# Performance work log

Measured on AMD Instinct MI355X. Metric: run time of the kernel, lower is better.

The kernel has to match this reference:

```python
import jax, jax.numpy as jnp
from jax import lax
import numpy as np

NPOINT = 1024   # S: number of sampled centroids
NSAMPLE = 32    # K: neighbors per centroid (unmasked ball query = k-nearest via argsort)


def _gather(p, i):
    # p: [B,N,C], i: [B,...] int -> [B,...,C]
    return jax.vmap(lambda pb, ib: pb[ib])(p, i)


def _fps(xyz, farthest_init, npoint):
    # Iterative farthest point sampling, faithful to the torch loop.
    B, N, _ = xyz.shape
    dist0 = jnp.full((B, N), 1e10, dtype=xyz.dtype)

    def step(carry, _):
        distance, farthest = carry
        centroid = jnp.take_along_axis(xyz, farthest[:, None, None], axis=1)  # [B,1,3]
        d = jnp.sum((xyz - centroid) ** 2, -1)          # [B,N]
        distance = jnp.minimum(distance, d)
        return (distance, jnp.argmax(distance, -1)), farthest

    _, cent = lax.scan(step, (dist0, farthest_init.astype(jnp.int32)), None, length=npoint)
    return cent.T  # [B, npoint]


def _sq_dist(src, dst):
    # src: [B,S,3], dst: [B,N,3] -> [B,S,N]
    return (jnp.sum(src ** 2, -1)[:, :, None]
            + jnp.sum(dst ** 2, -1)[:, None, :]
            - 2.0 * jnp.einsum('bsc,bnc->bsn', src, dst))


def setup_inputs() -> dict:
    key = jax.random.key(0)
    ks = jax.random.split(key, 6)
    B, N, C = 8, 4096, 6
    inp = {
        'xyz': jax.random.normal(ks[0], (B, N, 3), jnp.float32),
        'points': jax.random.normal(ks[1], (B, N, C), jnp.float32),
        'farthest_init': jax.random.randint(ks[2], (B,), 0, N),
    }
    dims = [C + 3, 64, 64, 128]
    for li in range(3):
        inp[f'w{li}'] = jax.random.normal(ks[3 + li], (dims[li + 1], dims[li]), jnp.float32) * 0.1
        inp[f'b{li}'] = jnp.zeros((dims[li + 1],), jnp.float32)
    return inp


def reference(xyz, points, farthest_init, w0, b0, w1, b1, w2, b2):
    fps_idx = _fps(xyz, farthest_init, NPOINT)            # [B,S]
    new_xyz = _gather(xyz, fps_idx)                       # [B,S,3]
    dist = _sq_dist(new_xyz, xyz)                         # [B,S,N]
    _, idx = lax.top_k(-dist, NSAMPLE)                    # k-nearest == argsort[:, :, :K]
    g_xyz = _gather(xyz, idx) - new_xyz[:, :, None, :]    # [B,S,K,3]
    g_pts = _gather(points, idx)                          # [B,S,K,C]
    h = jnp.concatenate([g_xyz, g_pts], axis=-1)          # [B,S,K,C+3]
    for w, b in ((w0, b0), (w1, b1), (w2, b2)):           # 1x1 conv MLP + relu
        h = jax.nn.relu(jnp.einsum('bskc,oc->bsko', h, w) + b)
    new_points = jnp.max(h, axis=2)                       # max-pool over K -> [B,S,128]
    return new_xyz, new_points
```

## Files before the change

### kernel.cpp

```cpp
#include <hip/hip_runtime.h>

#define INF_F 3.402823466e+38f
typedef unsigned long long u64;
typedef __attribute__((ext_vector_type(2))) float f32x2;

__device__ __forceinline__ float f_add(float a, float b){ return __fadd_rn(a,b); }
__device__ __forceinline__ float f_sub(float a, float b){ return __fsub_rn(a,b); }
__device__ __forceinline__ float f_mul(float a, float b){ return __fmul_rn(a,b); }

__device__ __forceinline__ f32x2 pk_add(f32x2 a, f32x2 b){ f32x2 d; asm("v_pk_add_f32 %0, %1, %2" : "=v"(d) : "v"(a), "v"(b)); return d; }
__device__ __forceinline__ f32x2 pk_mul(f32x2 a, f32x2 b){ f32x2 d; asm("v_pk_mul_f32 %0, %1, %2" : "=v"(d) : "v"(a), "v"(b)); return d; }
__device__ __forceinline__ f32x2 pk_fma(f32x2 a, f32x2 b, f32x2 c){ f32x2 d; asm("v_pk_fma_f32 %0, %1, %2, %3" : "=v"(d) : "v"(a), "v"(b), "v"(c)); return d; }

template<int CTRL>
__device__ __forceinline__ double dpp_d(double x) {
    u64 u = (u64)__double_as_longlong(x);
    int lo = __builtin_amdgcn_update_dpp(0, (int)(unsigned)u,        CTRL, 0xF, 0xF, true);
    int hi = __builtin_amdgcn_update_dpp(0, (int)(unsigned)(u>>32), CTRL, 0xF, 0xF, true);
    return __longlong_as_double((long long)(((u64)(unsigned)hi << 32) | (unsigned)lo));
}
template<int CTRL>
__device__ __forceinline__ float dpp_f(float x) {
    int r = __builtin_amdgcn_update_dpp(0, __float_as_int(x), CTRL, 0xF, 0xF, true);
    return __int_as_float(r);
}
__device__ __forceinline__ float swz16_f(float x) {
    return __int_as_float(__builtin_amdgcn_ds_swizzle(__float_as_int(x), 0x401F));
}
__device__ __forceinline__ double readlane_d(double x, int l) {
    u64 u = (u64)__double_as_longlong(x);
    int lo = __builtin_amdgcn_readlane((int)(unsigned)u,        l);
    int hi = __builtin_amdgcn_readlane((int)(unsigned)(u>>32), l);
    return __longlong_as_double((long long)(((u64)(unsigned)hi << 32) | (unsigned)lo));
}
__device__ __forceinline__ unsigned key_lo(double k) {
    return (unsigned)((u64)__double_as_longlong(k) & 0xFFFFFFFFull);
}
__device__ __forceinline__ double pack_key(float nd, unsigned low) {
    return __longlong_as_double((long long)(((u64)__float_as_uint(nd) << 32) | (u64)low));
}

__device__ __forceinline__ double wave_max_key(double k) {
    k = fmax(k, dpp_d<0xB1>(k));
    k = fmax(k, dpp_d<0x4E>(k));
    k = fmax(k, dpp_d<0x141>(k));
    k = fmax(k, dpp_d<0x140>(k));
    double a = readlane_d(k, 0),  b = readlane_d(k, 16);
    double c = readlane_d(k, 32), d = readlane_d(k, 48);
    return fmax(fmax(a, b), fmax(c, d));
}
__device__ __forceinline__ double wave_min_key(double k) {
    k = fmin(k, dpp_d<0xB1>(k));
    k = fmin(k, dpp_d<0x4E>(k));
    k = fmin(k, dpp_d<0x141>(k));
    k = fmin(k, dpp_d<0x140>(k));
    double a = readlane_d(k, 0),  b = readlane_d(k, 16);
    double c = readlane_d(k, 32), d = readlane_d(k, 48);
    return fmin(fmin(a, b), fmin(c, d));
}

__global__ __launch_bounds__(512, 1) void fps8_kernel(
    const float* __restrict__ xyz, const int* __restrict__ farthest_init,
    float* __restrict__ out_new_xyz)
{
    const int b    = blockIdx.x;
    const int tid  = threadIdx.x;
    const int lane = tid & 63;
    const int wid  = tid >> 6;

    __shared__ float4 sp[4096];
    __shared__ int    hist[1024];
    __shared__ double red[2][8];

    const float* xb = xyz + (size_t)b * 4096 * 3;
    for (int n = tid; n < 4096; n += 512)
        sp[n] = make_float4(xb[n*3+0], xb[n*3+1], xb[n*3+2], 0.0f);
    __syncthreads();

    f32x2 px[4], py[4], pz[4], d2a[4];
    #pragma unroll
    for (int jp = 0; jp < 4; ++jp) {
        const int n0 = (2*jp)*512 + tid, n1 = n0 + 512;
        float4 a = sp[n0], c = sp[n1];
        px[jp] = (f32x2){a.x, c.x};
        py[jp] = (f32x2){a.y, c.y};
        pz[jp] = (f32x2){a.z, c.z};
        d2a[jp] = (f32x2){1e10f, 1e10f};
    }

    int far = farthest_init[b];
    float4 cen = sp[far];
    float cx = cen.x, cy = cen.y, cz = cen.z;
    int p = 0;

    #pragma unroll 1
    for (int it = 0; it < 1024; ++it) {
        if (tid == 0) hist[it] = far;
        const f32x2 ncx = (f32x2){-cx, -cx};
        const f32x2 ncy = (f32x2){-cy, -cy};
        const f32x2 ncz = (f32x2){-cz, -cz};

        float nd[8];
        #pragma unroll
        for (int jp = 0; jp < 4; ++jp) {
            f32x2 dx = pk_add(px[jp], ncx);
            f32x2 dy = pk_add(py[jp], ncy);
            f32x2 dz = pk_add(pz[jp], ncz);
            f32x2 d2 = pk_add(pk_add(pk_mul(dx,dx), pk_mul(dy,dy)), pk_mul(dz,dz));
            float a0 = fminf(d2a[jp][0], d2[0]);
            float a1 = fminf(d2a[jp][1], d2[1]);
            d2a[jp][0] = a0; d2a[jp][1] = a1;
            nd[2*jp+0] = a0;
            nd[2*jp+1] = a1;
        }
        float vmax = fmaxf(fmaxf(fmaxf(nd[0], nd[1]), fmaxf(nd[2], nd[3])),
                           fmaxf(fmaxf(nd[4], nd[5]), fmaxf(nd[6], nd[7])));
        unsigned bestn = 0xFFFFFFFFu;
        #pragma unroll
        for (int j = 0; j < 8; ++j) {
            unsigned nj = (unsigned)(j*512 + tid);
            bestn = min(bestn, (nd[j] == vmax) ? nj : 0xFFFFFFFFu);
        }
        double wkey = wave_max_key(pack_key(vmax, 4095u - bestn));
        if (lane == 0) red[p][wid] = wkey;
        __syncthreads();
        const double g = fmax(fmax(fmax(red[p][0], red[p][1]), fmax(red[p][2], red[p][3])),
                              fmax(fmax(red[p][4], red[p][5]), fmax(red[p][6], red[p][7])));
        far = 4095 - (int)key_lo(g);
        float4 cc = sp[far];
        cx = cc.x; cy = cc.y; cz = cc.z;
        p ^= 1;
    }
    __syncthreads();
    #pragma unroll
    for (int q = 0; q < 2; ++q) {
        int s = q * 512 + tid;
        float4 cc = sp[hist[s]];
        float* o = out_new_xyz + ((size_t)b * 1024 + s) * 3;
        o[0] = cc.x; o[1] = cc.y; o[2] = cc.z;
    }
}

template<int G>
__device__ __forceinline__ double rebuild8(const double (&key)[64], double w) {
    const double DINF = __builtin_huge_val();
    double m = DINF;
    #pragma unroll
    for (int e = 0; e < 8; ++e) {
        double v = key[G*8+e];
        v = (v > w) ? v : DINF;
        m = fmin(m, v);
    }
    return m;
}

__global__ __launch_bounds__(256, 1) void knn_kernel(
    const float* __restrict__ xyz, const float* __restrict__ new_xyz,
    int* __restrict__ out_idx)
{
    const int tid  = threadIdx.x;
    const int lane = tid & 63;
    const int wid  = tid >> 6;
    const int blk  = blockIdx.x * 4 + wid;
    const int b    = blk >> 10;

    const float* xb = xyz + (size_t)b * 4096 * 3;
    const float* cp = new_xyz + (size_t)blk * 3;
    const float cx = cp[0], cy = cp[1], cz = cp[2];
    const float src2 = f_add(f_add(f_mul(cx,cx), f_mul(cy,cy)), f_mul(cz,cz));

    double key[64];
    #pragma unroll
    for (int j = 0; j < 64; ++j) {
        const int n = j * 64 + lane;
        const float* pt = xb + n * 3;
        float x = pt[0], y = pt[1], z = pt[2];
        float dst2 = f_add(f_add(f_mul(x,x), f_mul(y,y)), f_mul(z,z));
        float dot  = f_add(f_add(f_mul(cx,x), f_mul(cy,y)), f_mul(cz,z));
        float d = f_sub(f_add(src2, dst2), f_mul(2.0f, dot));
        key[j] = __longlong_as_double((long long)(((u64)__float_as_uint(d) << 32) | (u64)(unsigned)n));
    }

    double gm[8];
    #pragma unroll
    for (int g = 0; g < 8; ++g) {
        double m = key[g*8];
        #pragma unroll
        for (int e = 1; e < 8; ++e) m = fmin(m, key[g*8+e]);
        gm[g] = m;
    }

    double w = -1.0;
    int myidx = 0;
    #pragma unroll 1
    for (int t = 0; t < 32; ++t) {
        double lm = fmin(fmin(fmin(gm[0], gm[1]), fmin(gm[2], gm[3])),
                         fmin(fmin(gm[4], gm[5]), fmin(gm[6], gm[7])));
        double gmin = wave_min_key(lm);
        int n = (int)(unsigned)((u64)__double_as_longlong(gmin) & 0xFFFFFFFFull);
        if (lane == t) myidx = n;
        w = gmin;
        const int gs = __builtin_amdgcn_readfirstlane(n >> 9);
        switch (gs) {
            case 0: gm[0] = rebuild8<0>(key, w); break;
            case 1: gm[1] = rebuild8<1>(key, w); break;
            case 2: gm[2] = rebuild8<2>(key, w); break;
            case 3: gm[3] = rebuild8<3>(key, w); break;
            case 4: gm[4] = rebuild8<4>(key, w); break;
            case 5: gm[5] = rebuild8<5>(key, w); break;
            case 6: gm[6] = rebuild8<6>(key, w); break;
            case 7: gm[7] = rebuild8<7>(key, w); break;
        }
    }
    if (lane < 32) out_idx[(size_t)blk * 32 + lane] = myidx;
}

__global__ __launch_bounds__(256, 1) void mlp_kernel(
    const float* __restrict__ xyz, const float* __restrict__ points,
    const int* __restrict__ knn_idx,
    const float* __restrict__ w0, const float* __restrict__ b0,
    const float* __restrict__ w1, const float* __restrict__ b1,
    const float* __restrict__ w2, const float* __restrict__ b2,
    const float* __restrict__ new_xyz, float* __restrict__ out_np)
{
    const int tid = threadIdx.x;
    const int k   = tid & 31;
    const int gs  = blockIdx.x * 8 + (tid >> 5);
    const int b   = gs >> 10;
    const int n   = knn_idx[(size_t)gs * 32 + k];

    const float cx = new_xyz[gs*3+0], cy = new_xyz[gs*3+1], cz = new_xyz[gs*3+2];
    const float* pxyz = xyz + ((size_t)b * 4096 + n) * 3;
    float h0[9];
    h0[0] = pxyz[0] - cx;
    h0[1] = pxyz[1] - cy;
    h0[2] = pxyz[2] - cz;
    const float* pp = points + ((size_t)b * 4096 + n) * 6;
    #pragma unroll
    for (int c = 0; c < 6; ++c) h0[3 + c] = pp[c];

    f32x2 h1p[32];
    #pragma unroll
    for (int o = 0; o < 64; o += 2) {
        float accA = b0[o], accB = b0[o+1];
        #pragma unroll
        for (int c = 0; c < 9; ++c) {
            accA = fmaf(h0[c], w0[o*9+c],     accA);
            accB = fmaf(h0[c], w0[(o+1)*9+c], accB);
        }
        h1p[o>>1] = (f32x2){fmaxf(accA, 0.0f), fmaxf(accB, 0.0f)};
    }

    const f32x2* w1v = (const f32x2*)w1;
    f32x2 h2p[32];
    #pragma unroll
    for (int o = 0; o < 64; o += 2) {
        f32x2 accA = (f32x2){b1[o],   0.0f};
        f32x2 accB = (f32x2){b1[o+1], 0.0f};
        #pragma unroll
        for (int i = 0; i < 32; ++i) {
            accA = pk_fma(h1p[i], w1v[o*32+i],     accA);
            accB = pk_fma(h1p[i], w1v[(o+1)*32+i], accB);
        }
        h2p[o>>1] = (f32x2){fmaxf(accA[0]+accA[1], 0.0f), fmaxf(accB[0]+accB[1], 0.0f)};
    }

    const f32x2* w2v = (const f32x2*)w2;
    float* outp = out_np + (size_t)gs * 128;
    for (int og = 0; og < 4; ++og) {
        float keep = 0.0f;
        for (int o2 = 0; o2 < 32; ++o2) {
            const int o = og * 32 + o2;
            f32x2 acc = (f32x2){b2[o], 0.0f};
            #pragma unroll
            for (int i = 0; i < 32; ++i) acc = pk_fma(h2p[i], w2v[o*32+i], acc);
            float m = fmaxf(acc[0] + acc[1], 0.0f);
            m = fmaxf(m, dpp_f<0xB1>(m));
            m = fmaxf(m, dpp_f<0x4E>(m));
            m = fmaxf(m, dpp_f<0x141>(m));
            m = fmaxf(m, dpp_f<0x140>(m));
            m = fmaxf(m, swz16_f(m));
            keep = (k == o2) ? m : keep;
        }
        outp[og * 32 + k] = keep;
    }
}

__global__ __launch_bounds__(256) void knn_mlp_kernel(
    const float* __restrict__ xyz, const float* __restrict__ points,
    const float* __restrict__ w0, const float* __restrict__ b0,
    const float* __restrict__ w1, const float* __restrict__ b1,
    const float* __restrict__ w2, const float* __restrict__ b2,
    const float* __restrict__ new_xyz, float* __restrict__ out_np)
{
    const int blk    = blockIdx.x;
    const int b      = blk >> 7;
    const int s_base = (blk & 127) * 8;
    const int tid    = threadIdx.x;
    const int lane   = tid & 63;
    const int wid    = tid >> 6;

    __shared__ float sx[4096], sy[4096], sz[4096];
    __shared__ float cent[8][3];
    __shared__ int   idxbuf[8][32];

    const float* xb = xyz + (size_t)b * 4096 * 3;
    for (int n = tid; n < 4096; n += 256) {
        sx[n] = xb[n*3+0]; sy[n] = xb[n*3+1]; sz[n] = xb[n*3+2];
    }
    if (tid < 24) ((float*)cent)[tid] = new_xyz[((size_t)b * 1024 + s_base) * 3 + tid];
    __syncthreads();

    for (int si = 0; si < 2; ++si) {
        const int sl = wid * 2 + si;
        const float cx = cent[sl][0], cy = cent[sl][1], cz = cent[sl][2];
        const float src2 = f_add(f_add(f_mul(cx,cx), f_mul(cy,cy)), f_mul(cz,cz));
        float d[64];
        #pragma unroll
        for (int j = 0; j < 64; ++j) {
            int n = j * 64 + lane;
            float x = sx[n], y = sy[n], z = sz[n];
            float dst2 = f_add(f_add(f_mul(x,x), f_mul(y,y)), f_mul(z,z));
            float dot  = f_add(f_add(f_mul(cx,x), f_mul(cy,y)), f_mul(cz,z));
            d[j] = f_sub(f_add(src2, dst2), f_mul(2.0f, dot));
        }
        int myg  = 0;
        int prev = -1;
        for (int t = 0; t < 32; ++t) {
            float bv = INF_F; int bi = 0x7fffffff;
            #pragma unroll
            for (int j = 0; j < 64; ++j) {
                int n = j * 64 + lane;
                if (n == prev) d[j] = INF_F;
                float v = d[j];
                if (v < bv) { bv = v; bi = n; }
            }
            #pragma unroll
            for (int m = 1; m < 64; m <<= 1) {
                float ov = __shfl_xor(bv, m);
                int   oi = __shfl_xor(bi, m);
                if (ov < bv || (ov == bv && oi < bi)) { bv = ov; bi = oi; }
            }
            if (lane == t) myg = bi;
            prev = bi;
        }
        if (lane < 32) idxbuf[sl][lane] = myg;
    }
    __syncthreads();

    const int k   = tid & 31;
    const int sl2 = tid >> 5;
    const int s   = s_base + sl2;
    const int n   = idxbuf[sl2][k];

    const float cx = cent[sl2][0], cy = cent[sl2][1], cz = cent[sl2][2];
    float h0[9];
    h0[0] = sx[n] - cx;
    h0[1] = sy[n] - cy;
    h0[2] = sz[n] - cz;
    const float* pp = points + ((size_t)b * 4096 + n) * 6;
    #pragma unroll
    for (int c = 0; c < 6; ++c) h0[3 + c] = pp[c];

    float h1[64];
    #pragma unroll
    for (int o = 0; o < 64; ++o) {
        float acc = b0[o];
        #pragma unroll
        for (int c = 0; c < 9; ++c) acc = fmaf(h0[c], w0[o*9+c], acc);
        h1[o] = fmaxf(acc, 0.0f);
    }
    float h2[64];
    #pragma unroll
    for (int o = 0; o < 64; ++o) {
        float acc = b1[o];
        #pragma unroll
        for (int c = 0; c < 64; ++c) acc = fmaf(h1[c], w1[o*64+c], acc);
        h2[o] = fmaxf(acc, 0.0f);
    }
    float* outp = out_np + ((size_t)b * 1024 + s) * 128;
    for (int og = 0; og < 4; ++og) {
        float keep = 0.0f;
        for (int o2 = 0; o2 < 32; ++o2) {
            const int o = og * 32 + o2;
            float acc = b2[o];
            #pragma unroll
            for (int c = 0; c < 64; ++c) acc = fmaf(h2[c], w2[o*64+c], acc);
            float m = fmaxf(acc, 0.0f);
            #pragma unroll
            for (int mm = 1; mm < 32; mm <<= 1)
                m = fmaxf(m, __shfl_xor(m, mm));
            keep = (k == o2) ? m : keep;
        }
        outp[og * 32 + k] = keep;
    }
}

extern "C" void kernel_launch(void* const* d_in, const int* in_sizes, int n_in,
                              void* d_out, int out_size, void* d_ws, size_t ws_size,
                              hipStream_t stream) {
    const float* xyz           = (const float*)d_in[0];
    const float* points        = (const float*)d_in[1];
    const int*   farthest_init = (const int*)  d_in[2];
    const float* w0 = (const float*)d_in[3];
    const float* b0 = (const float*)d_in[4];
    const float* w1 = (const float*)d_in[5];
    const float* b1 = (const float*)d_in[6];
    const float* w2 = (const float*)d_in[7];
    const float* b2 = (const float*)d_in[8];

    float* out        = (float*)d_out;
    float* new_xyz    = out;
    float* new_points = out + 8 * 1024 * 3;

    fps8_kernel<<<8, 512, 0, stream>>>(xyz, farthest_init, new_xyz);

    if (ws_size >= (size_t)(8192 * 32 * sizeof(int))) {
        int* knn_idx = (int*)d_ws;
        knn_kernel<<<2048, 256, 0, stream>>>(xyz, new_xyz, knn_idx);
        mlp_kernel<<<1024, 256, 0, stream>>>(xyz, points, knn_idx,
                                             w0, b0, w1, b1, w2, b2,
                                             new_xyz, new_points);
    } else {
        knn_mlp_kernel<<<1024, 256, 0, stream>>>(xyz, points, w0, b0, w1, b1, w2, b2,
                                                 new_xyz, new_points);
    }
}
```

Baseline: 881.2 us.

## Replace FPS per-iteration barrier with LDS spin-wait slots and 4 waves

Reworks the farthest point sampling kernel to run 4 waves of 256 threads, each holding 16 points, instead of 8 waves of 512. The per-iteration __syncthreads reduction is replaced by a per-iteration LDS slot array, pre-filled with a poison value, that each wave polls until all four wave maxima are published. The aim is to remove block-barrier latency from the serial 1024-step loop. In exchange each thread carries more registers and ALU work per step, and correctness depends on LDS visibility ordering under volatile spinning with no fences, plus the poison value never colliding with a real key.

```diff
diff --git a/kernel.cpp b/kernel.cpp
--- a/kernel.cpp
+++ b/kernel.cpp
@@ -3,6 +3,8 @@
 #define INF_F 3.402823466e+38f
 typedef unsigned long long u64;
 typedef __attribute__((ext_vector_type(2))) float f32x2;
+
+#define SLOT_POISON 0xAAAAAAAAAAAAAAAAull
 
 __device__ __forceinline__ float f_add(float a, float b){ return __fadd_rn(a,b); }
 __device__ __forceinline__ float f_sub(float a, float b){ return __fsub_rn(a,b); }
@@ -59,7 +61,7 @@
     return fmin(fmin(a, b), fmin(c, d));
 }
 
-__global__ __launch_bounds__(512, 1) void fps8_kernel(
+__global__ __launch_bounds__(256, 1) void fps_spin_kernel(
     const float* __restrict__ xyz, const int* __restrict__ farthest_init,
     float* __restrict__ out_new_xyz)
 {
@@ -70,17 +72,18 @@
 
     __shared__ float4 sp[4096];
     __shared__ int    hist[1024];
-    __shared__ double red[2][8];
+    __shared__ u64    slot[1024][4];
 
     const float* xb = xyz + (size_t)b * 4096 * 3;
-    for (int n = tid; n < 4096; n += 512)
+    for (int n = tid; n < 4096; n += 256)
         sp[n] = make_float4(xb[n*3+0], xb[n*3+1], xb[n*3+2], 0.0f);
+    for (int i = tid; i < 4096; i += 256) ((u64*)slot)[i] = SLOT_POISON;
     __syncthreads();
 
-    f32x2 px[4], py[4], pz[4], d2a[4];
-    #pragma unroll
-    for (int jp = 0; jp < 4; ++jp) {
-        const int n0 = (2*jp)*512 + tid, n1 = n0 + 512;
+    f32x2 px[8], py[8], pz[8], d2a[8];
+    #pragma unroll
+    for (int jp = 0; jp < 8; ++jp) {
+        const int n0 = (2*jp)*256 + tid, n1 = n0 + 256;
         float4 a = sp[n0], c = sp[n1];
         px[jp] = (f32x2){a.x, c.x};
         py[jp] = (f32x2){a.y, c.y};
@@ -91,7 +94,6 @@
     int far = farthest_init[b];
     float4 cen = sp[far];
     float cx = cen.x, cy = cen.y, cz = cen.z;
-    int p = 0;
 
     #pragma unroll 1
     for (int it = 0; it < 1024; ++it) {
@@ -100,9 +102,9 @@
         const f32x2 ncy = (f32x2){-cy, -cy};
         const f32x2 ncz = (f32x2){-cz, -cz};
 
-        float nd[8];
-        #pragma unroll
-        for (int jp = 0; jp < 4; ++jp) {
+        float nd[16];
+        #pragma unroll
+        for (int jp = 0; jp < 8; ++jp) {
             f32x2 dx = pk_add(px[jp], ncx);
             f32x2 dy = pk_add(py[jp], ncy);
             f32x2 dz = pk_add(pz[jp], ncz);
@@ -113,30 +115,41 @@
             nd[2*jp+0] = a0;
             nd[2*jp+1] = a1;
         }
-        float vmax = fmaxf(fmaxf(fmaxf(nd[0], nd[1]), fmaxf(nd[2], nd[3])),
-                           fmaxf(fmaxf(nd[4], nd[5]), fmaxf(nd[6], nd[7])));
+        float m01 = fmaxf(nd[0], nd[1]),   m23 = fmaxf(nd[2], nd[3]);
+        float m45 = fmaxf(nd[4], nd[5]),   m67 = fmaxf(nd[6], nd[7]);
+        float m89 = fmaxf(nd[8], nd[9]),   mAB = fmaxf(nd[10], nd[11]);
+        float mCD = fmaxf(nd[12], nd[13]), mEF = fmaxf(nd[14], nd[15]);
+        float vmax = fmaxf(fmaxf(fmaxf(m01, m23), fmaxf(m45, m67)),
+                           fmaxf(fmaxf(m89, mAB), fmaxf(mCD, mEF)));
         unsigned bestn = 0xFFFFFFFFu;
         #pragma unroll
-        for (int j = 0; j < 8; ++j) {
-            unsigned nj = (unsigned)(j*512 + tid);
+        for (int j = 0; j < 16; ++j) {
+            unsigned nj = (unsigned)(j*256 + tid);
             bestn = min(bestn, (nd[j] == vmax) ? nj : 0xFFFFFFFFu);
         }
         double wkey = wave_max_key(pack_key(vmax, 4095u - bestn));
-        if (lane == 0) red[p][wid] = wkey;
-        __syncthreads();
-        const double g = fmax(fmax(fmax(red[p][0], red[p][1]), fmax(red[p][2], red[p][3])),
-                              fmax(fmax(red[p][4], red[p][5]), fmax(red[p][6], red[p][7])));
+
+        if (lane == 0) slot[it][wid] = (u64)__double_as_longlong(wkey);
+        volatile const u64* s = &slot[it][0];
+        u64 k0, k1, k2, k3;
+        do {
+            k0 = s[0]; k1 = s[1]; k2 = s[2]; k3 = s[3];
+        } while (k0 == SLOT_POISON || k1 == SLOT_POISON ||
+                 k2 == SLOT_POISON || k3 == SLOT_POISON);
+        const double g = fmax(fmax(__longlong_as_double((long long)k0),
+                                   __longlong_as_double((long long)k1)),
+                              fmax(__longlong_as_double((long long)k2),
+                                   __longlong_as_double((long long)k3)));
         far = 4095 - (int)key_lo(g);
         float4 cc = sp[far];
         cx = cc.x; cy = cc.y; cz = cc.z;
-        p ^= 1;
     }
     __syncthreads();
     #pragma unroll
-    for (int q = 0; q < 2; ++q) {
-        int s = q * 512 + tid;
-        float4 cc = sp[hist[s]];
-        float* o = out_new_xyz + ((size_t)b * 1024 + s) * 3;
+    for (int q = 0; q < 4; ++q) {
+        int s2 = q * 256 + tid;
+        float4 cc = sp[hist[s2]];
+        float* o = out_new_xyz + ((size_t)b * 1024 + s2) * 3;
         o[0] = cc.x; o[1] = cc.y; o[2] = cc.z;
     }
 }
@@ -413,7 +426,7 @@
     float* new_xyz    = out;
     float* new_points = out + 8 * 1024 * 3;
 
-    fps8_kernel<<<8, 512, 0, stream>>>(xyz, farthest_init, new_xyz);
+    fps_spin_kernel<<<8, 256, 0, stream>>>(xyz, farthest_init, new_xyz);
 
     if (ws_size >= (size_t)(8192 * 32 * sizeof(int))) {
         int* knn_idx = (int*)d_ws;
```

Result: slower. 991.1 us (+12.5%).
